# Performance work log

Hardware: AMD Instinct MI355X
Metric: run time of the kernel (lower is better)

Reference implementation:

```python
import jax, jax.numpy as jnp
import numpy as np

N = 50000      # nodes
E = 600000     # edges
DIN = 518      # object_feature_dim
D = 128        # node_embedding_dim
ED = 32        # edge_embedding_dim
R = 26         # num_relations
SD = 32        # scene_embedding_dim
NEG_SLOPE = 0.2


def setup_inputs() -> dict:
    key = jax.random.key(0)
    ks = jax.random.split(key, 26)
    g = lambda k, s: (jax.random.normal(k, s, jnp.float32) * 0.05)
    return {
        "x": jax.random.normal(ks[0], (N, DIN), jnp.float32),
        "edge_index": jax.random.randint(ks[1], (2, E), 0, N),
        "edge_attr": jax.random.randint(ks[2], (E,), 0, R),
        # node encoder MLP
        "W1": g(ks[3], (DIN, 256)), "b1": jnp.zeros((256,), jnp.float32),
        "W2": g(ks[4], (256, D)),   "b2": jnp.zeros((D,), jnp.float32),
        # relation embedding table
        "rel_emb": g(ks[5], (R, ED)),
        # GATConv 1 (heads=1): shared lin, attention vectors, edge lin, bias
        "lin1": g(ks[6], (D, D)), "att_src1": g(ks[7], (D,)), "att_dst1": g(ks[8], (D,)),
        "att_edge1": g(ks[9], (D,)), "line1": g(ks[10], (ED, D)), "bias1": jnp.zeros((D,), jnp.float32),
        # GATConv 2
        "lin2": g(ks[11], (D, D)), "att_src2": g(ks[12], (D,)), "att_dst2": g(ks[13], (D,)),
        "att_edge2": g(ks[14], (D,)), "line2": g(ks[15], (ED, D)), "bias2": jnp.zeros((D,), jnp.float32),
        # readout MLP
        "Wr1": g(ks[16], (D, 64)), "br1": jnp.zeros((64,), jnp.float32),
        "Wr2": g(ks[17], (64, SD)), "br2": jnp.zeros((SD,), jnp.float32),
    }


def _gat_layer(h, e2, src2, dst2, W, a_src, a_dst, a_edge, We, bias):
    """PyG GATConv (heads=1, concat) with edge_dim, self-loops already appended."""
    hp = h @ W                       # [N, D]
    ep = e2 @ We                     # [E+N, D]
    # per-edge attention logits
    logit = (hp @ a_src)[src2] + (hp @ a_dst)[dst2] + ep @ a_edge  # [E+N]
    logit = jax.nn.leaky_relu(logit, NEG_SLOPE)
    # segment softmax over destination nodes
    mx = jax.ops.segment_max(logit, dst2, num_segments=N)
    ex = jnp.exp(logit - mx[dst2])
    den = jax.ops.segment_sum(ex, dst2, num_segments=N)
    alpha = ex / (den[dst2] + 1e-16)
    # weighted scatter-add aggregation
    out = jax.ops.segment_sum(hp[src2] * alpha[:, None], dst2, num_segments=N)
    return out + bias


def reference(x, edge_index, edge_attr, W1, b1, W2, b2, rel_emb,
              lin1, att_src1, att_dst1, att_edge1, line1, bias1,
              lin2, att_src2, att_dst2, att_edge2, line2, bias2,
              Wr1, br1, Wr2, br2):
    # node encoder MLP
    h = jax.nn.relu(x @ W1 + b1) @ W2 + b2            # [N, D]
    # learned edge vectors
    e = rel_emb[edge_attr]                             # [E, ED]
    src, dst = edge_index[0], edge_index[1]
    # add self-loops; fill_value='mean' -> mean of incoming edge attrs per node
    esum = jax.ops.segment_sum(e, dst, num_segments=N)
    cnt = jax.ops.segment_sum(jnp.ones((e.shape[0], 1), e.dtype), dst, num_segments=N)
    eloop = esum / jnp.maximum(cnt, 1.0)
    loop = jnp.arange(N)
    src2 = jnp.concatenate([src, loop])
    dst2 = jnp.concatenate([dst, loop])
    e2 = jnp.concatenate([e, eloop], axis=0)
    # two GAT layers with ReLU
    h = jax.nn.relu(_gat_layer(h, e2, src2, dst2, lin1, att_src1, att_dst1, att_edge1, line1, bias1))
    h = jax.nn.relu(_gat_layer(h, e2, src2, dst2, lin2, att_src2, att_dst2, att_edge2, line2, bias2))
    # global mean pool (single graph)
    g = jnp.mean(h, axis=0, keepdims=True)             # [1, D]
    # readout MLP
    return jax.nn.relu(g @ Wr1 + br1) @ Wr2 + br2      # [1, SD]
```

## Files before the change

kernel.cpp:

```cpp
#include <hip/hip_runtime.h>
#include <hip/hip_bf16.h>

#define NN   50000
#define EE   600000
#define DINK 518
#define KP1  576
#define MP   50048
#define DD   128
#define NEG_SLOPE 0.2f
#define CAP  64

typedef short bf16x8 __attribute__((ext_vector_type(8)));
typedef float f32x4 __attribute__((ext_vector_type(4)));

typedef const __attribute__((address_space(1))) void* gp1_t;
typedef __attribute__((address_space(3))) void* lp3_t;

__device__ __forceinline__ void load_lds16(const void* g, void* l) {
  __builtin_amdgcn_global_load_lds((gp1_t)g, (lp3_t)l, 16, 0, 0);
}

__device__ __forceinline__ unsigned short f2bf(float f) {
  union { float f; unsigned u; } q; q.f = f;
  unsigned u = q.u + 0x7FFFu + ((q.u >> 16) & 1u);
  return (unsigned short)(u >> 16);
}
__device__ __forceinline__ float bflo(unsigned u) {
  union { unsigned u; float f; } q; q.u = u << 16; return q.f;
}
__device__ __forceinline__ float bfhi(unsigned u) {
  union { unsigned u; float f; } q; q.u = u & 0xFFFF0000u; return q.f;
}

template<bool OUT_BF16, bool RELU, bool HASBIAS, bool DOTS>
__global__ __launch_bounds__(256) void gemm_mfma(
    const unsigned short* __restrict__ A, const unsigned short* __restrict__ BT,
    const float* __restrict__ bias, void* __restrict__ Cout,
    int M, int Ncols, int K,
    const float* __restrict__ att_src, const float* __restrict__ att_dst,
    float* __restrict__ ssrc, float* __restrict__ sdst) {
  __shared__ short As[128][64];
  __shared__ short Bs[128][64];
  __shared__ float sp[128], dp[128];
  const int tid = threadIdx.x;
  const int lane = tid & 63;
  const int wid = tid >> 6;
  const int wr = wid >> 1, wc = wid & 1;
  const int bm = blockIdx.x * 128;
  const int bn = blockIdx.y * 128;
  const int ar = tid >> 3;
  const int ac = (tid & 7) * 8;

  f32x4 acc[4][4] = {};

  for (int k0 = 0; k0 < K; k0 += 64) {
#pragma unroll
    for (int i = 0; i < 4; i++) {
      int row = ar + i * 32;
      int acs = ac ^ ((row & 7) << 3);
      load_lds16(A + (size_t)(bm + row) * K + k0 + acs, &As[row][ac]);
    }
#pragma unroll
    for (int i = 0; i < 4; i++) {
      int row = ar + i * 32;
      int acs = ac ^ ((row & 7) << 3);
      load_lds16(BT + (size_t)(bn + row) * K + k0 + acs, &Bs[row][ac]);
    }
    __syncthreads();
#pragma unroll
    for (int ks = 0; ks < 2; ks++) {
      bf16x8 af[4], bfm[4];
#pragma unroll
      for (int f = 0; f < 4; f++) {
        int ra = wr * 64 + f * 16 + (lane & 15);
        af[f] = *(const bf16x8*)&As[ra][(ks * 32 + (lane >> 4) * 8) ^ ((ra & 7) << 3)];
      }
#pragma unroll
      for (int f = 0; f < 4; f++) {
        int rb = wc * 64 + f * 16 + (lane & 15);
        bfm[f] = *(const bf16x8*)&Bs[rb][(ks * 32 + (lane >> 4) * 8) ^ ((rb & 7) << 3)];
      }
#pragma unroll
      for (int i = 0; i < 4; i++)
#pragma unroll
        for (int j = 0; j < 4; j++)
          acc[i][j] = __builtin_amdgcn_mfma_f32_16x16x32_bf16(af[i], bfm[j], acc[i][j], 0, 0, 0);
    }
    __syncthreads();
  }

  const int col0 = bn + wc * 64 + (lane & 15);
  const int row0 = bm + wr * 64 + (lane >> 4) * 4;
#pragma unroll
  for (int i = 0; i < 4; i++) {
#pragma unroll
    for (int jf = 0; jf < 4; jf++) {
      int col = col0 + jf * 16;
      float bv = HASBIAS ? bias[col] : 0.f;
#pragma unroll
      for (int j = 0; j < 4; j++) {
        int row = row0 + i * 16 + j;
        if (row < M) {
          float v = acc[i][jf][j] + bv;
          if (RELU) v = fmaxf(v, 0.f);
          if (OUT_BF16)
            ((unsigned short*)Cout)[(size_t)row * Ncols + col] = f2bf(v);
          else
            ((float*)Cout)[(size_t)row * Ncols + col] = v;
        }
      }
    }
  }

  if (DOTS) {
    float as_[4], ad_[4], bv_[4];
#pragma unroll
    for (int jf = 0; jf < 4; jf++) {
      int col = col0 + jf * 16;
      as_[jf] = att_src[col];
      ad_[jf] = att_dst[col];
      bv_[jf] = HASBIAS ? bias[col] : 0.f;
    }
    float ps[4][4], pd[4][4];
#pragma unroll
    for (int i = 0; i < 4; i++) {
#pragma unroll
      for (int j = 0; j < 4; j++) {
        float s = 0.f, d = 0.f;
#pragma unroll
        for (int jf = 0; jf < 4; jf++) {
          float vv = acc[i][jf][j] + bv_[jf];
          s += vv * as_[jf];
          d += vv * ad_[jf];
        }
#pragma unroll
        for (int off = 1; off < 16; off <<= 1) {
          s += __shfl_xor(s, off);
          d += __shfl_xor(d, off);
        }
        ps[i][j] = s; pd[i][j] = d;
      }
    }
    if (wc == 0 && (lane & 15) == 0) {
#pragma unroll
      for (int i = 0; i < 4; i++)
#pragma unroll
        for (int j = 0; j < 4; j++) {
          int r = wr * 64 + i * 16 + (lane >> 4) * 4 + j;
          sp[r] = ps[i][j]; dp[r] = pd[i][j];
        }
    }
    __syncthreads();
    if (wc == 1 && (lane & 15) == 0) {
#pragma unroll
      for (int i = 0; i < 4; i++)
#pragma unroll
        for (int j = 0; j < 4; j++) {
          int r = wr * 64 + i * 16 + (lane >> 4) * 4 + j;
          sp[r] += ps[i][j]; dp[r] += pd[i][j];
        }
    }
    __syncthreads();
    if (tid < 128) {
      int gr = bm + tid;
      if (gr < M) { ssrc[gr] = sp[tid]; sdst[gr] = dp[tid]; }
    }
  }
}

__global__ __launch_bounds__(256) void gemm1_fused(
    const float* __restrict__ x, const unsigned short* __restrict__ BT,
    const float* __restrict__ bias, unsigned short* __restrict__ Cout) {
  __shared__ short As[64][68];
  __shared__ short Bs[128][64];
  const int tid = threadIdx.x;
  const int lane = tid & 63;
  const int wid = tid >> 6;
  const int bm = blockIdx.x * 64;
  const int bn = blockIdx.y * 128;
  const int br = tid >> 3;
  const int bc = (tid & 7) * 8;
  const int rlane = lane >> 5;
  const int klane = (lane & 31) * 2;

  f32x4 acc[4][2] = {};

  for (int k0 = 0; k0 < KP1; k0 += 64) {
#pragma unroll
    for (int i = 0; i < 4; i++) {
      int row = br + i * 32;
      int bcs = bc ^ ((row & 7) << 3);
      load_lds16(BT + (size_t)(bn + row) * KP1 + k0 + bcs, &Bs[row][bc]);
    }
    float2 v[8];
    const int kk = k0 + klane;
    const bool kok = (kk < DINK);
#pragma unroll
    for (int i = 0; i < 8; i++) {
      int grow = bm + wid * 16 + i * 2 + rlane;
      v[i] = make_float2(0.f, 0.f);
      if (kok && grow < NN) v[i] = *(const float2*)&x[(size_t)grow * DINK + kk];
    }
#pragma unroll
    for (int i = 0; i < 8; i++) {
      int rl = wid * 16 + i * 2 + rlane;
      unsigned pk;
      asm("v_cvt_pk_bf16_f32 %0, %1, %2" : "=v"(pk) : "v"(v[i].x), "v"(v[i].y));
      *(unsigned*)&As[rl][klane] = pk;
    }
    __syncthreads();
#pragma unroll
    for (int ks = 0; ks < 2; ks++) {
      bf16x8 af[4], bfm[2];
#pragma unroll
      for (int f = 0; f < 4; f++)
        af[f] = *(const bf16x8*)&As[f * 16 + (lane & 15)][ks * 32 + (lane >> 4) * 8];
#pragma unroll
      for (int f = 0; f < 2; f++) {
        int rb = wid * 32 + f * 16 + (lane & 15);
        bfm[f] = *(const bf16x8*)&Bs[rb][(ks * 32 + (lane >> 4) * 8) ^ ((rb & 7) << 3)];
      }
#pragma unroll
      for (int i = 0; i < 4; i++)
#pragma unroll
        for (int j = 0; j < 2; j++)
          acc[i][j] = __builtin_amdgcn_mfma_f32_16x16x32_bf16(af[i], bfm[j], acc[i][j], 0, 0, 0);
    }
    __syncthreads();
  }

  const int col0 = bn + wid * 32 + (lane & 15);
  const int row0 = bm + (lane >> 4) * 4;
#pragma unroll
  for (int i = 0; i < 4; i++) {
#pragma unroll
    for (int jf = 0; jf < 2; jf++) {
      int col = col0 + jf * 16;
      float bv = bias[col];
#pragma unroll
      for (int j = 0; j < 4; j++) {
        int row = row0 + i * 16 + j;
        if (row < NN) {
          float v2 = fmaxf(acc[i][jf][j] + bv, 0.f);
          Cout[(size_t)row * 256 + col] = f2bf(v2);
        }
      }
    }
  }
}

__device__ __forceinline__ void convT_body(const float* __restrict__ W,
                                           unsigned short* __restrict__ WT,
                                           int K, int Ncols, int Kpad, int t) {
  int n = t / Kpad, k = t % Kpad;
  float v = (k < K) ? W[(size_t)k * Ncols + n] : 0.f;
  WT[(size_t)n * Kpad + k] = f2bf(v);
}

__global__ __launch_bounds__(256) void prep_kernel(
    const float* __restrict__ W1, const float* __restrict__ W2,
    const float* __restrict__ l1, const float* __restrict__ l2,
    const float* __restrict__ le1, const float* __restrict__ le2,
    const float* __restrict__ ae1, const float* __restrict__ ae2,
    const float* __restrict__ rel_emb, const float* __restrict__ b2,
    unsigned short* __restrict__ W1T, unsigned short* __restrict__ W2L1T,
    unsigned short* __restrict__ l2T, float* __restrict__ tables,
    float* __restrict__ b2l1, int* __restrict__ cnt, float* __restrict__ g) {
  const int b = blockIdx.x, tid = threadIdx.x;
  if (b < 576) { convT_body(W1, W1T, DINK, 256, KP1, b * 256 + tid); return; }
  if (b < 640) { convT_body(l2, l2T, 128, 128, 128, (b - 576) * 256 + tid); return; }
  if (b < 642) {
    const int layer = b - 640;
    const float* line = layer ? le2 : le1;
    const float* ae   = layer ? ae2 : ae1;
    __shared__ float ve[32];
    if (tid < 32) {
      float s = 0.f;
      for (int d = 0; d < 128; d++) s += line[tid * 128 + d] * ae[d];
      ve[tid] = s;
    }
    __syncthreads();
    if (tid < 26) {
      float s = 0.f;
      for (int j = 0; j < 32; j++) s += rel_emb[tid * 32 + j] * ve[j];
      tables[layer * 32 + tid] = s;
    }
    return;
  }
  if (b < 770) {
    const int n = b - 642;
    __shared__ float lc[128];
    if (tid < 128) lc[tid] = l1[(size_t)tid * 128 + n];
    __syncthreads();
    float s = 0.f;
    const float* wrow = W2 + (size_t)tid * 128;
    for (int j = 0; j < 128; j++) s += wrow[j] * lc[j];
    W2L1T[(size_t)n * 256 + tid] = f2bf(s);
    if (tid == 0) {
      float bb = 0.f;
      for (int j = 0; j < 128; j++) bb += b2[j] * lc[j];
      b2l1[n] = bb;
    }
    return;
  }
  {
    const int zb = b - 770;
    int i = zb * 256 + tid;
    if (i < NN) cnt[i] = 0;
    if (zb == 0 && tid < 128) g[tid] = 0.f;
  }
}

__global__ void bucket_kernel(const int* __restrict__ src, const int* __restrict__ dst,
                              const int* __restrict__ attr, int* __restrict__ cnt,
                              int* __restrict__ cpack, int E) {
  int e = blockIdx.x * blockDim.x + threadIdx.x;
  if (e >= E) return;
  int d = dst[e];
  int p = atomicAdd(&cnt[d], 1);
  if (p < CAP) cpack[d * CAP + p] = (src[e] << 5) | attr[e];
}

__global__ __launch_bounds__(256) void gat_gather_kernel(
    const int* __restrict__ cnt, const int* __restrict__ cpack,
    const float* __restrict__ table,
    const float* __restrict__ ssrc, const float* __restrict__ sdst,
    const unsigned short* __restrict__ hp, const float* __restrict__ bias,
    unsigned short* __restrict__ hout, int n) {
  __shared__ float exs[4][2][CAP];
  __shared__ int   srcs[4][2][CAP];
  const int wid = threadIdx.x >> 6, lane = threadIdx.x & 63;
  const int half = lane >> 5, hlane = lane & 31;
  const int node = ((blockIdx.x * blockDim.x + threadIdx.x) >> 6) * 2 + half;
  const bool valid = node < n;
  int deg = valid ? cnt[node] : 0;
  if (deg > CAP) deg = CAP;
  const int j0 = node * CAP;
  const float sd = valid ? sdst[node] : 0.f;
  float den = 0.f, esum = 0.f;
  for (int k = hlane; k < deg; k += 32) {
    int pk_ = cpack[j0 + k];
    int s = pk_ >> 5;
    float t = table[pk_ & 31];
    float l = ssrc[s] + sd + t;
    l = (l > 0.f) ? l : NEG_SLOPE * l;
    float ex = expf(l);
    exs[wid][half][k] = ex; srcs[wid][half][k] = s * DD;
    den += ex; esum += t;
  }
#pragma unroll
  for (int off = 16; off; off >>= 1) {
    den += __shfl_xor(den, off);
    esum += __shfl_xor(esum, off);
  }
  float tl = esum / fmaxf((float)deg, 1.f);
  float ll = (valid ? ssrc[node] : 0.f) + sd + tl;
  ll = (ll > 0.f) ? ll : NEG_SLOPE * ll;
  float exl = expf(ll);
  den += exl;
  const float inv = 1.f / (den + 1e-16f);
  const int c = hlane * 4;
  float a0, a1, a2, a3;
  {
    uint2 w = valid ? *(const uint2*)&hp[(size_t)node * DD + c] : make_uint2(0, 0);
    float a = exl * inv;
    a0 = a * bflo(w.x); a1 = a * bfhi(w.x);
    a2 = a * bflo(w.y); a3 = a * bfhi(w.y);
  }
  int k = 0;
  for (; k + 8 <= deg; k += 8) {
    uint2 w[8]; float a[8];
#pragma unroll
    for (int q = 0; q < 8; q++) {
      a[q] = exs[wid][half][k + q] * inv;
      w[q] = *(const uint2*)&hp[(size_t)(srcs[wid][half][k + q] + c)];
    }
#pragma unroll
    for (int q = 0; q < 8; q++) {
      a0 += a[q] * bflo(w[q].x); a1 += a[q] * bfhi(w[q].x);
      a2 += a[q] * bflo(w[q].y); a3 += a[q] * bfhi(w[q].y);
    }
  }
  for (; k + 4 <= deg; k += 4) {
    uint2 w[4]; float a[4];
#pragma unroll
    for (int q = 0; q < 4; q++) {
      a[q] = exs[wid][half][k + q] * inv;
      w[q] = *(const uint2*)&hp[(size_t)(srcs[wid][half][k + q] + c)];
    }
#pragma unroll
    for (int q = 0; q < 4; q++) {
      a0 += a[q] * bflo(w[q].x); a1 += a[q] * bfhi(w[q].x);
      a2 += a[q] * bflo(w[q].y); a3 += a[q] * bfhi(w[q].y);
    }
  }
  for (; k < deg; k++) {
    float aq = exs[wid][half][k] * inv;
    uint2 w = *(const uint2*)&hp[(size_t)(srcs[wid][half][k] + c)];
    a0 += aq * bflo(w.x); a1 += aq * bfhi(w.x);
    a2 += aq * bflo(w.y); a3 += aq * bfhi(w.y);
  }
  if (valid) {
    a0 = fmaxf(a0 + bias[c], 0.f);
    a1 = fmaxf(a1 + bias[c + 1], 0.f);
    a2 = fmaxf(a2 + bias[c + 2], 0.f);
    a3 = fmaxf(a3 + bias[c + 3], 0.f);
    uint2 o;
    o.x = (unsigned)f2bf(a0) | ((unsigned)f2bf(a1) << 16);
    o.y = (unsigned)f2bf(a2) | ((unsigned)f2bf(a3) << 16);
    *(uint2*)&hout[(size_t)node * DD + c] = o;
  }
}

__global__ void pool_kernel(const unsigned short* __restrict__ h, float* __restrict__ g, int n) {
  __shared__ float sh[128];
  int tid = threadIdx.x;
  int cp = tid & 63, half = tid >> 6;
  float sx = 0.f, sy = 0.f;
  for (int r = blockIdx.x * 4 + half; r < n; r += gridDim.x * 4) {
    unsigned w = *(const unsigned*)&h[(size_t)r * DD + cp * 2];
    sx += bflo(w); sy += bfhi(w);
  }
  if (half == 0) { sh[cp * 2] = sx; sh[cp * 2 + 1] = sy; }
  __syncthreads();
  if (half == 1) { sh[cp * 2] += sx; sh[cp * 2 + 1] += sy; }
  __syncthreads();
  if (half == 2) { sh[cp * 2] += sx; sh[cp * 2 + 1] += sy; }
  __syncthreads();
  if (half == 3) {
    atomicAdd(&g[cp * 2], sh[cp * 2] + sx);
    atomicAdd(&g[cp * 2 + 1], sh[cp * 2 + 1] + sy);
  }
}

__global__ void readout_kernel(const float* __restrict__ g, const float* __restrict__ Wr1,
                               const float* __restrict__ br1, const float* __restrict__ Wr2,
                               const float* __restrict__ br2, float* __restrict__ out,
                               float inv_n) {
  __shared__ float gl[128];
  __shared__ float m[64];
  int t = threadIdx.x;
  gl[t] = g[t] * inv_n;
  gl[t + 64] = g[t + 64] * inv_n;
  __syncthreads();
  {
    float acc = br1[t];
    for (int c = 0; c < 128; c++) acc += gl[c] * Wr1[c * 64 + t];
    m[t] = fmaxf(acc, 0.f);
  }
  __syncthreads();
  if (t < 32) {
    float acc = br2[t];
    for (int j = 0; j < 64; j++) acc += m[j] * Wr2[j * 32 + t];
    out[t] = acc;
  }
}

extern "C" void kernel_launch(void* const* d_in, const int* in_sizes, int n_in,
                              void* d_out, int out_size, void* d_ws, size_t ws_size,
                              hipStream_t stream) {
  const float* x     = (const float*)d_in[0];
  const int*   ei    = (const int*)d_in[1];
  const int*   eattr = (const int*)d_in[2];
  const float* W1 = (const float*)d_in[3];
  const float* b1 = (const float*)d_in[4];
  const float* W2 = (const float*)d_in[5];
  const float* b2 = (const float*)d_in[6];
  const float* rel_emb = (const float*)d_in[7];
  const float* lin[2]      = {(const float*)d_in[8],  (const float*)d_in[14]};
  const float* att_src[2]  = {(const float*)d_in[9],  (const float*)d_in[15]};
  const float* att_dst[2]  = {(const float*)d_in[10], (const float*)d_in[16]};
  const float* att_edge[2] = {(const float*)d_in[11], (const float*)d_in[17]};
  const float* line[2]     = {(const float*)d_in[12], (const float*)d_in[18]};
  const float* bias[2]     = {(const float*)d_in[13], (const float*)d_in[19]};
  const float* Wr1 = (const float*)d_in[20];
  const float* br1 = (const float*)d_in[21];
  const float* Wr2 = (const float*)d_in[22];
  const float* br2 = (const float*)d_in[23];
  float* out = (float*)d_out;

  const int* srcv = ei;
  const int* dstv = ei + EE;

  char* wsb = (char*)d_ws;
  unsigned short* hA  = (unsigned short*)(wsb + 0);
  unsigned short* hp  = (unsigned short*)(wsb + 12900000);
  unsigned short* hB  = (unsigned short*)(wsb + 25900000);
  unsigned short* mid = (unsigned short*)(wsb + 38800000);
  unsigned short* W1T   = (unsigned short*)(wsb + 64600000);
  unsigned short* W2L1T = (unsigned short*)(wsb + 64900000);
  unsigned short* lin2T = (unsigned short*)(wsb + 65040000);
  int* cnt     = (int*)(wsb + 65300008);
  float* ssrc  = (float*)(wsb + 68100008);
  float* sdst  = (float*)(wsb + 68300008);
  float* tables = (float*)(wsb + 68502056);
  float* g      = (float*)(wsb + 68502312);
  float* b2l1   = (float*)(wsb + 68502824);
  int* cpack    = (int*)(wsb + 70000000);

  dim3 blk(256);

  prep_kernel<<<dim3(966), blk, 0, stream>>>(
      W1, W2, lin[0], lin[1], line[0], line[1], att_edge[0], att_edge[1],
      rel_emb, b2, W1T, W2L1T, lin2T, tables, b2l1, cnt, g);
  gemm1_fused<<<dim3(782, 2), blk, 0, stream>>>(x, W1T, b1, mid);

  bucket_kernel<<<dim3((EE + 255) / 256), blk, 0, stream>>>(srcv, dstv, eattr, cnt, cpack, EE);

  gemm_mfma<true, false, true, true><<<dim3(391, 1), blk, 0, stream>>>(
      mid, W2L1T, b2l1, hp, NN, 128, 256, att_src[0], att_dst[0], ssrc, sdst);
  gat_gather_kernel<<<dim3((NN / 2 * 64 + 255) / 256), blk, 0, stream>>>(
      cnt, cpack, tables, ssrc, sdst, hp, bias[0], hB, NN);
  gemm_mfma<true, false, false, true><<<dim3(391, 1), blk, 0, stream>>>(
      hB, lin2T, nullptr, hp, NN, 128, 128, att_src[1], att_dst[1], ssrc, sdst);
  gat_gather_kernel<<<dim3((NN / 2 * 64 + 255) / 256), blk, 0, stream>>>(
      cnt, cpack, tables + 32, ssrc, sdst, hp, bias[1], hA, NN);

  pool_kernel<<<dim3(256), blk, 0, stream>>>(hA, g, NN);
  readout_kernel<<<1, 64, 0, stream>>>(g, Wr1, br1, Wr2, br2, out, 1.0f / NN);
}
```

Baseline: 227.0 us.

## Fuse encoder GEMM1 and GEMM2 with attention scores into one kernel

Merges the first encoder GEMM (x@W1, ReLU) with the second GEMM (mid@W2·lin1) and the attention-score dot products into a single kernel. Each block now computes all 256 mid columns for 64 rows and keeps them in LDS instead of writing the 50000x256 bf16 intermediate to global memory and reading it back. This removes one launch and the global round-trip of the intermediate. In exchange, LDS use per block rises sharply (about 70KB), which lowers occupancy. The grid also halves to 782 blocks, and the B-tile swizzle is dropped, which can add LDS bank conflicts.

```diff
diff --git a/kernel.cpp b/kernel.cpp
--- a/kernel.cpp
+++ b/kernel.cpp
@@ -5,7 +5,6 @@
 #define EE   600000
 #define DINK 518
 #define KP1  576
-#define MP   50048
 #define DD   128
 #define NEG_SLOPE 0.2f
 #define CAP  64
@@ -168,30 +167,31 @@
   }
 }
 
-__global__ __launch_bounds__(256) void gemm1_fused(
-    const float* __restrict__ x, const unsigned short* __restrict__ BT,
-    const float* __restrict__ bias, unsigned short* __restrict__ Cout) {
+__global__ __launch_bounds__(256) void enc_fused(
+    const float* __restrict__ x, const unsigned short* __restrict__ W1T,
+    const float* __restrict__ b1, const unsigned short* __restrict__ W2L1T,
+    const float* __restrict__ b2l1,
+    const float* __restrict__ att_src, const float* __restrict__ att_dst,
+    unsigned short* __restrict__ hp, float* __restrict__ ssrc,
+    float* __restrict__ sdst) {
   __shared__ short As[64][68];
-  __shared__ short Bs[128][64];
+  __shared__ short Bs[256][64];
+  __shared__ short midT[64][264];
+  __shared__ float sp4[4][64], dp4[4][64];
   const int tid = threadIdx.x;
   const int lane = tid & 63;
   const int wid = tid >> 6;
   const int bm = blockIdx.x * 64;
-  const int bn = blockIdx.y * 128;
   const int br = tid >> 3;
   const int bc = (tid & 7) * 8;
   const int rlane = lane >> 5;
   const int klane = (lane & 31) * 2;
 
-  f32x4 acc[4][2] = {};
-
+  f32x4 acc[4][4] = {};
   for (int k0 = 0; k0 < KP1; k0 += 64) {
 #pragma unroll
-    for (int i = 0; i < 4; i++) {
-      int row = br + i * 32;
-      int bcs = bc ^ ((row & 7) << 3);
-      load_lds16(BT + (size_t)(bn + row) * KP1 + k0 + bcs, &Bs[row][bc]);
-    }
+    for (int i = 0; i < 8; i++)
+      load_lds16(W1T + (size_t)(br + i * 32) * KP1 + k0 + bc, &Bs[br + i * 32][bc]);
     float2 v[8];
     const int kk = k0 + klane;
     const bool kok = (kk < DINK);
@@ -211,40 +211,103 @@
     __syncthreads();
 #pragma unroll
     for (int ks = 0; ks < 2; ks++) {
-      bf16x8 af[4], bfm[2];
+      bf16x8 af[4], bfm[4];
 #pragma unroll
       for (int f = 0; f < 4; f++)
         af[f] = *(const bf16x8*)&As[f * 16 + (lane & 15)][ks * 32 + (lane >> 4) * 8];
 #pragma unroll
-      for (int f = 0; f < 2; f++) {
-        int rb = wid * 32 + f * 16 + (lane & 15);
-        bfm[f] = *(const bf16x8*)&Bs[rb][(ks * 32 + (lane >> 4) * 8) ^ ((rb & 7) << 3)];
+      for (int c = 0; c < 4; c++)
+        bfm[c] = *(const bf16x8*)&Bs[wid * 64 + c * 16 + (lane & 15)][ks * 32 + (lane >> 4) * 8];
+#pragma unroll
+      for (int f = 0; f < 4; f++)
+#pragma unroll
+        for (int c = 0; c < 4; c++)
+          acc[f][c] = __builtin_amdgcn_mfma_f32_16x16x32_bf16(af[f], bfm[c], acc[f][c], 0, 0, 0);
+    }
+    __syncthreads();
+  }
+  {
+    const int col0 = wid * 64 + (lane & 15);
+    const int r0 = (lane >> 4) * 4;
+#pragma unroll
+    for (int c = 0; c < 4; c++) {
+      int col = col0 + c * 16;
+      float bv = b1[col];
+#pragma unroll
+      for (int f = 0; f < 4; f++)
+#pragma unroll
+        for (int j = 0; j < 4; j++) {
+          float vv = fmaxf(acc[f][c][j] + bv, 0.f);
+          midT[f * 16 + r0 + j][col] = (short)f2bf(vv);
+        }
+    }
+  }
+  __syncthreads();
+
+  f32x4 acc2[4][2] = {};
+  for (int t2 = 0; t2 < 4; ++t2) {
+    const int k0 = t2 * 64;
+#pragma unroll
+    for (int i = 0; i < 4; i++)
+      load_lds16(W2L1T + (size_t)(br + i * 32) * 256 + k0 + bc, &Bs[br + i * 32][bc]);
+    __syncthreads();
+#pragma unroll
+    for (int ks = 0; ks < 2; ks++) {
+      bf16x8 af[4], bfm[2];
+#pragma unroll
+      for (int f = 0; f < 4; f++)
+        af[f] = *(const bf16x8*)&midT[f * 16 + (lane & 15)][k0 + ks * 32 + (lane >> 4) * 8];
+#pragma unroll
+      for (int cf = 0; cf < 2; cf++)
+        bfm[cf] = *(const bf16x8*)&Bs[wid * 32 + cf * 16 + (lane & 15)][ks * 32 + (lane >> 4) * 8];
+#pragma unroll
+      for (int f = 0; f < 4; f++)
+#pragma unroll
+        for (int cf = 0; cf < 2; cf++)
+          acc2[f][cf] = __builtin_amdgcn_mfma_f32_16x16x32_bf16(af[f], bfm[cf], acc2[f][cf], 0, 0, 0);
+    }
+    __syncthreads();
+  }
+  {
+    const int col0 = wid * 32 + (lane & 15);
+    const int r0 = (lane >> 4) * 4;
+    float as_[2], ad_[2], bv_[2];
+#pragma unroll
+    for (int cf = 0; cf < 2; cf++) {
+      int col = col0 + cf * 16;
+      as_[cf] = att_src[col]; ad_[cf] = att_dst[col]; bv_[cf] = b2l1[col];
+    }
+#pragma unroll
+    for (int f = 0; f < 4; f++) {
+#pragma unroll
+      for (int j = 0; j < 4; j++) {
+        int row = bm + f * 16 + r0 + j;
+        float s = 0.f, d = 0.f;
+#pragma unroll
+        for (int cf = 0; cf < 2; cf++) {
+          float vv = acc2[f][cf][j] + bv_[cf];
+          s += vv * as_[cf]; d += vv * ad_[cf];
+          if (row < NN)
+            hp[(size_t)row * DD + col0 + cf * 16] = f2bf(vv);
+        }
+#pragma unroll
+        for (int off = 1; off < 16; off <<= 1) {
+          s += __shfl_xor(s, off);
+          d += __shfl_xor(d, off);
+        }
+        if ((lane & 15) == 0) {
+          sp4[wid][f * 16 + r0 + j] = s;
+          dp4[wid][f * 16 + r0 + j] = d;
+        }
       }
-#pragma unroll
-      for (int i = 0; i < 4; i++)
-#pragma unroll
-        for (int j = 0; j < 2; j++)
-          acc[i][j] = __builtin_amdgcn_mfma_f32_16x16x32_bf16(af[i], bfm[j], acc[i][j], 0, 0, 0);
-    }
-    __syncthreads();
-  }
-
-  const int col0 = bn + wid * 32 + (lane & 15);
-  const int row0 = bm + (lane >> 4) * 4;
-#pragma unroll
-  for (int i = 0; i < 4; i++) {
-#pragma unroll
-    for (int jf = 0; jf < 2; jf++) {
-      int col = col0 + jf * 16;
-      float bv = bias[col];
-#pragma unroll
-      for (int j = 0; j < 4; j++) {
-        int row = row0 + i * 16 + j;
-        if (row < NN) {
-          float v2 = fmaxf(acc[i][jf][j] + bv, 0.f);
-          Cout[(size_t)row * 256 + col] = f2bf(v2);
-        }
-      }
+    }
+  }
+  __syncthreads();
+  if (tid < 64) {
+    int gr = bm + tid;
+    if (gr < NN) {
+      ssrc[gr] = sp4[0][tid] + sp4[1][tid] + sp4[2][tid] + sp4[3][tid];
+      sdst[gr] = dp4[0][tid] + dp4[1][tid] + dp4[2][tid] + dp4[3][tid];
     }
   }
 }
@@ -486,7 +549,6 @@
   unsigned short* hA  = (unsigned short*)(wsb + 0);
   unsigned short* hp  = (unsigned short*)(wsb + 12900000);
   unsigned short* hB  = (unsigned short*)(wsb + 25900000);
-  unsigned short* mid = (unsigned short*)(wsb + 38800000);
   unsigned short* W1T   = (unsigned short*)(wsb + 64600000);
   unsigned short* W2L1T = (unsigned short*)(wsb + 64900000);
   unsigned short* lin2T = (unsigned short*)(wsb + 65040000);
@@ -503,12 +565,12 @@
   prep_kernel<<<dim3(966), blk, 0, stream>>>(
       W1, W2, lin[0], lin[1], line[0], line[1], att_edge[0], att_edge[1],
       rel_emb, b2, W1T, W2L1T, lin2T, tables, b2l1, cnt, g);
-  gemm1_fused<<<dim3(782, 2), blk, 0, stream>>>(x, W1T, b1, mid);
+
+  enc_fused<<<dim3(782), blk, 0, stream>>>(
+      x, W1T, b1, W2L1T, b2l1, att_src[0], att_dst[0], hp, ssrc, sdst);
 
   bucket_kernel<<<dim3((EE + 255) / 256), blk, 0, stream>>>(srcv, dstv, eattr, cnt, cpack, EE);
 
-  gemm_mfma<true, false, true, true><<<dim3(391, 1), blk, 0, stream>>>(
-      mid, W2L1T, b2l1, hp, NN, 128, 256, att_src[0], att_dst[0], ssrc, sdst);
   gat_gather_kernel<<<dim3((NN / 2 * 64 + 255) / 256), blk, 0, stream>>>(
       cnt, cpack, tables, ssrc, sdst, hp, bias[0], hB, NN);
   gemm_mfma<true, false, false, true><<<dim3(391, 1), blk, 0, stream>>>(
```

Result: faster. 212.5 us (-6.4%).
